# Optimization experiments

Measured on AMD Instinct MI355X. Metric: run time of the kernel, lower is better.

## Reference

```python
import jax, jax.numpy as jnp
import numpy as np

LN_EPS = 1e-5

def layer_norm(x, g, b):
    mu = jnp.mean(x, axis=-1, keepdims=True)
    var = jnp.mean(jnp.square(x - mu), axis=-1, keepdims=True)
    return (x - mu) * jax.lax.rsqrt(var + LN_EPS) * g + b

def ternary_quant(w):
    # BitNet b1.58-style ternary quantization with straight-through estimator
    scale = 1.0 / jnp.clip(jnp.mean(jnp.abs(w)), 1e-5)
    wq = jnp.clip(jnp.round(w * scale), -1.0, 1.0) / scale
    return w + jax.lax.stop_gradient(wq - w)

def setup_inputs() -> dict:
    key = jax.random.key(0)
    ks = jax.random.split(key, 3)
    dim, hidden = 1024, 4096
    B, S = 8, 1024
    x = jax.random.normal(ks[0], (B, S, dim), dtype=jnp.float32)
    w1 = jax.random.normal(ks[1], (hidden, dim), dtype=jnp.float32) * 0.02
    w2 = jax.random.normal(ks[2], (dim, hidden), dtype=jnp.float32) * 0.02
    return {
        "x": x,
        "ln1_g": jnp.ones((dim,), jnp.float32), "ln1_b": jnp.zeros((dim,), jnp.float32),
        "w1": w1, "b1": jnp.zeros((hidden,), jnp.float32),
        "ln2_g": jnp.ones((hidden,), jnp.float32), "ln2_b": jnp.zeros((hidden,), jnp.float32),
        "w2": w2, "b2": jnp.zeros((dim,), jnp.float32),
    }

def reference(x, ln1_g, ln1_b, w1, b1, ln2_g, ln2_b, w2, b2):
    h = layer_norm(x, ln1_g, ln1_b)
    h = jnp.einsum('bsd,hd->bsh', h, ternary_quant(w1)) + b1  # [B,S,hidden]
    h = jax.nn.gelu(h, approximate=False)  # nn.GELU default is exact erf
    h = layer_norm(h, ln2_g, ln2_b)
    out = jnp.einsum('bsh,dh->bsd', h, ternary_quant(w2)) + b2  # [B,S,dim]
    return out
```

## Files before the change

kernel.cpp:

```cpp
#include <hip/hip_runtime.h>
#include <cstdint>
#include <cstddef>

#define DIM   1024
#define HID   4096
#define MROWS 8192

typedef __attribute__((ext_vector_type(8))) __bf16 bf16x8;
typedef __attribute__((ext_vector_type(4))) float  f32x4;
typedef __attribute__((ext_vector_type(4))) int    i32x4;

__device__ __forceinline__ unsigned short f2bf(float f) {
  unsigned int u = __float_as_uint(f);
  u += 0x7fffu + ((u >> 16) & 1u);
  return (unsigned short)(u >> 16);
}
__device__ __forceinline__ float bf2f(unsigned int lo16) {
  return __uint_as_float(lo16 << 16);
}

__device__ __forceinline__ float fast_gelu(float v) {
  float u = v * (0.79788456080286536f + 0.035677408136300125f * v * v);
  float e = __builtin_amdgcn_exp2f(u * 2.8853900817779268f);
  float r = __builtin_amdgcn_rcpf(e + 1.0f);
  return v - v * r;
}

__device__ __forceinline__ void gld16(const void* g, void* l) {
  auto* gp = reinterpret_cast<__attribute__((address_space(1))) unsigned int*>(
      reinterpret_cast<uintptr_t>(g));
  auto* lp = reinterpret_cast<__attribute__((address_space(3))) unsigned int*>(
      reinterpret_cast<uintptr_t>(l));
  __builtin_amdgcn_global_load_lds(gp, lp, 16, 0, 0);
}

__device__ __forceinline__ void wave_reduce2(float& a, float& b) {
#pragma unroll
  for (int off = 32; off > 0; off >>= 1) {
    a += __shfl_xor(a, off, 64);
    b += __shfl_xor(b, off, 64);
  }
}
__device__ __forceinline__ float wave_reduce_max(float m) {
#pragma unroll
  for (int off = 32; off > 0; off >>= 1) m = fmaxf(m, __shfl_xor(m, off, 64));
  return m;
}

__device__ __forceinline__ void block_reduce2(float& a, float& b, int tid) {
  __shared__ float red[8];
  __syncthreads();
  wave_reduce2(a, b);
  if ((tid & 63) == 0) { red[tid >> 6] = a; red[4 + (tid >> 6)] = b; }
  __syncthreads();
  a = red[0] + red[1] + red[2] + red[3];
  b = red[4] + red[5] + red[6] + red[7];
}

__global__ __launch_bounds__(256)
void prep_kernel(const float* __restrict__ w1, const float* __restrict__ w2,
                 float* __restrict__ part,
                 const float* __restrict__ x, const float* __restrict__ g,
                 const float* __restrict__ b, unsigned int* __restrict__ xn8,
                 float* __restrict__ invs) {
  int tid = threadIdx.x;
  int bid = blockIdx.x;
  if (bid < 2048) {
    const float* w = (bid < 1024) ? w1 : w2;
    int blk = bid & 1023;
    const float4* base = (const float4*)w + (size_t)blk * 1024;
    float s = 0.f;
#pragma unroll
    for (int i = 0; i < 4; ++i) {
      float4 v = base[tid + i * 256];
      s += fabsf(v.x) + fabsf(v.y) + fabsf(v.z) + fabsf(v.w);
    }
#pragma unroll
    for (int off = 32; off > 0; off >>= 1) s += __shfl_xor(s, off, 64);
    __shared__ float red[4];
    if ((tid & 63) == 0) red[tid >> 6] = s;
    __syncthreads();
    if (tid == 0) part[bid] = red[0] + red[1] + red[2] + red[3];
  } else {
    const int row  = (bid - 2048) * 4 + (tid >> 6);
    const int lane = tid & 63;
    const float4* xr = (const float4*)(x + (size_t)row * DIM);
    const float4* g4 = (const float4*)g;
    const float4* b4 = (const float4*)b;
    float4 v[4];
    float s = 0.f, ss = 0.f;
#pragma unroll
    for (int p = 0; p < 4; ++p) {
      v[p] = xr[lane + 64 * p];
      s  += v[p].x + v[p].y + v[p].z + v[p].w;
      ss += v[p].x * v[p].x + v[p].y * v[p].y + v[p].z * v[p].z + v[p].w * v[p].w;
    }
    wave_reduce2(s, ss);
    float mu  = s * (1.0f / DIM);
    float var = ss * (1.0f / DIM) - mu * mu;
    float rs  = rsqrtf(var + 1e-5f);
    float n[4][4];
    float amax = 0.f;
#pragma unroll
    for (int p = 0; p < 4; ++p) {
      float4 gg = g4[lane + 64 * p];
      float4 bb = b4[lane + 64 * p];
      n[p][0] = (v[p].x - mu) * rs * gg.x + bb.x;
      n[p][1] = (v[p].y - mu) * rs * gg.y + bb.y;
      n[p][2] = (v[p].z - mu) * rs * gg.z + bb.z;
      n[p][3] = (v[p].w - mu) * rs * gg.w + bb.w;
#pragma unroll
      for (int c = 0; c < 4; ++c) amax = fmaxf(amax, fabsf(n[p][c]));
    }
    amax = wave_reduce_max(amax);
    float sc, iv;
    if (amax < 1e-20f) { sc = 0.f; iv = 0.f; }
    else               { sc = 127.0f / amax; iv = amax * (1.0f / 127.0f); }
    if (lane == 0) invs[row] = iv;
    unsigned int* dst = xn8 + (size_t)row * 256;
#pragma unroll
    for (int p = 0; p < 4; ++p) {
      unsigned r = 0;
#pragma unroll
      for (int c = 0; c < 4; ++c) {
        int q = (int)rintf(n[p][c] * sc);
        r |= ((unsigned)q & 0xffu) << (8 * c);
      }
      dst[lane + 64 * p] = r;
    }
  }
}

__global__ __launch_bounds__(256)
void quant_kernel(const float* __restrict__ part,
                  const float* __restrict__ w1, unsigned int* __restrict__ q1,
                  const float* __restrict__ w2, unsigned short* __restrict__ q2,
                  const float* __restrict__ g2, const float* __restrict__ b2,
                  const float* __restrict__ bias2,
                  float* __restrict__ Sg, float* __restrict__ Cb,
                  float* __restrict__ scal) {
  int bid = blockIdx.x, tid = threadIdx.x;
  const int lane = tid & 63;
  const float4* psrc = (const float4*)(part + ((bid < 512) ? 0 : 1024));
  float a = 0.f, dummy = 0.f;
#pragma unroll
  for (int p = 0; p < 4; ++p) {
    float4 pv = psrc[lane + 64 * p];
    a += pv.x + pv.y + pv.z + pv.w;
  }
  wave_reduce2(a, dummy);
  float mean = fmaxf(a * (1.0f / 4194304.0f), 1e-5f);
  float sc = 1.0f / mean;

  if (bid < 512) {
    if (bid == 0 && tid == 0) scal[0] = mean;
    const int n4 = 1048576;
    int i = bid * 256 + tid;
    for (; i < n4; i += 512 * 256) {
      float4 v = ((const float4*)w1)[i];
      int t0 = (int)fminf(fmaxf(rintf(v.x * sc), -1.f), 1.f);
      int t1 = (int)fminf(fmaxf(rintf(v.y * sc), -1.f), 1.f);
      int t2 = (int)fminf(fmaxf(rintf(v.z * sc), -1.f), 1.f);
      int t3 = (int)fminf(fmaxf(rintf(v.w * sc), -1.f), 1.f);
      unsigned r = ((unsigned)t0 & 0xffu) | (((unsigned)t1 & 0xffu) << 8) |
                   (((unsigned)t2 & 0xffu) << 16) | (((unsigned)t3 & 0xffu) << 24);
      q1[i] = r;
    }
  } else {
    const int d = bid - 512;
    if (d == 0 && tid == 0) scal[1] = mean;
    const float4* wr = (const float4*)(w2 + (size_t)d * HID);
    const float4* g4 = (const float4*)g2;
    const float4* b4 = (const float4*)b2;
    uint2* qr = (uint2*)(q2 + (size_t)d * HID);
    float s1 = 0.f, s2 = 0.f;
#pragma unroll
    for (int i = 0; i < 4; ++i) {
      int idx = tid + 256 * i;
      float4 wv = wr[idx], gv = g4[idx], bv = b4[idx];
      float t0 = fminf(fmaxf(rintf(wv.x * sc), -1.f), 1.f);
      float t1 = fminf(fmaxf(rintf(wv.y * sc), -1.f), 1.f);
      float t2 = fminf(fmaxf(rintf(wv.z * sc), -1.f), 1.f);
      float t3 = fminf(fmaxf(rintf(wv.w * sc), -1.f), 1.f);
      s1 += gv.x * t0 + gv.y * t1 + gv.z * t2 + gv.w * t3;
      s2 += bv.x * t0 + bv.y * t1 + bv.z * t2 + bv.w * t3;
      uint2 r;
      r.x = (unsigned)f2bf(t0 * gv.x) | ((unsigned)f2bf(t1 * gv.y) << 16);
      r.y = (unsigned)f2bf(t2 * gv.z) | ((unsigned)f2bf(t3 * gv.w) << 16);
      qr[idx] = r;
    }
    block_reduce2(s1, s2, tid);
    if (tid == 0) {
      Sg[d] = mean * s1;
      Cb[d] = mean * s2 + bias2[d];
    }
  }
}

__global__ __launch_bounds__(256)
void rowstats_kernel(const unsigned short* __restrict__ h,
                     const float* __restrict__ meanp,
                     float2* __restrict__ murs) {
  const int row  = blockIdx.x * 4 + (threadIdx.x >> 6);
  const int lane = threadIdx.x & 63;
  const uint4* hr = (const uint4*)(h + (size_t)row * HID);
  float s = 0.f, ss = 0.f;
#pragma unroll
  for (int p = 0; p < 8; ++p) {
    uint4 pk = hr[lane + 64 * p];
    const unsigned int* pu = (const unsigned int*)&pk;
#pragma unroll
    for (int j = 0; j < 4; ++j) {
      float lo = bf2f(pu[j] & 0xffffu);
      float hi = __uint_as_float(pu[j] & 0xffff0000u);
      s += lo + hi; ss += lo * lo + hi * hi;
    }
  }
  wave_reduce2(s, ss);
  if (lane == 0) {
    float mu  = s * (1.0f / HID);
    float var = ss * (1.0f / HID) - mu * mu;
    float rs  = rsqrtf(var + 1e-5f);
    murs[row] = make_float2(rs * meanp[1], -rs * mu);
  }
}

__global__ __launch_bounds__(256)
void gemm1_i8(const unsigned char* __restrict__ A,
              const unsigned char* __restrict__ B,
              unsigned short* __restrict__ H,
              const float* __restrict__ wscale_ptr,
              const float* __restrict__ invs,
              const float* __restrict__ bias) {
  __shared__ unsigned char sA[128 * 64];
  __shared__ unsigned char sB[128 * 64];

  const int tid  = threadIdx.x;
  const int lane = tid & 63;
  const int wave = tid >> 6;
  const int wm   = wave & 1;
  const int wn   = wave >> 1;

  const int nbx  = gridDim.x;
  const int id   = blockIdx.y * nbx + blockIdx.x;
  const int xcd  = id & 7;
  const int slot = id >> 3;
  const int bandsPerXcd = gridDim.y >> 3;
  const int band = xcd * bandsPerXcd + slot / nbx;
  const int col  = slot - (slot / nbx) * nbx;
  const int bm   = band * 128;
  const int bn   = col * 128;

  const int csw = ((tid & 3) ^ ((tid >> 3) & 3)) * 16;
  const unsigned char* Ab = A + (size_t)(bm + (tid >> 2)) * 1024 + csw;
  const unsigned char* Bb = B + (size_t)(bn + (tid >> 2)) * 1024 + csw;

  i32x4 acc[4][4] = {};

  const int rowA = (wm * 64 + (lane & 15)) * 64;
  const int rowB = (wn * 64 + (lane & 15)) * 64;
  const int kc = (((lane >> 4) ^ ((lane >> 1) & 3))) * 16;

  for (int k0 = 0; k0 < 1024; k0 += 64) {
    gld16(Ab + k0,              sA + tid * 16);
    gld16(Ab + 64 * 1024 + k0,  sA + 4096 + tid * 16);
    gld16(Bb + k0,              sB + tid * 16);
    gld16(Bb + 64 * 1024 + k0,  sB + 4096 + tid * 16);
    __syncthreads();

    i32x4 af[4], bfr[4];
#pragma unroll
    for (int i = 0; i < 4; ++i) af[i]  = *(const i32x4*)(sA + rowA + i * 1024 + kc);
#pragma unroll
    for (int j = 0; j < 4; ++j) bfr[j] = *(const i32x4*)(sB + rowB + j * 1024 + kc);
#pragma unroll
    for (int i = 0; i < 4; ++i)
#pragma unroll
      for (int j = 0; j < 4; ++j)
        acc[i][j] = __builtin_amdgcn_mfma_i32_16x16x64_i8(af[i], bfr[j], acc[i][j], 0, 0, 0);
    __syncthreads();
  }

  const float wscale = *wscale_ptr;
  float bv[4];
#pragma unroll
  for (int j = 0; j < 4; ++j) bv[j] = bias[bn + wn * 64 + j * 16 + (lane & 15)];
#pragma unroll
  for (int i = 0; i < 4; ++i) {
    const int m0 = bm + wm * 64 + i * 16 + ((lane >> 4) << 2);
    float asc[4];
#pragma unroll
    for (int r = 0; r < 4; ++r) asc[r] = wscale * invs[m0 + r];
#pragma unroll
    for (int j = 0; j < 4; ++j) {
      const int n = bn + wn * 64 + j * 16 + (lane & 15);
#pragma unroll
      for (int r = 0; r < 4; ++r) {
        float v = fast_gelu((float)acc[i][j][r] * asc[r] + bv[j]);
        H[(size_t)(m0 + r) * HID + n] = f2bf(v);
      }
    }
  }
}

template <int MODE, int MT, int KK>
__global__ __launch_bounds__(256)
void gemm_bt(const unsigned short* __restrict__ A,
             const unsigned short* __restrict__ B,
             void* __restrict__ Cv,
             const float* __restrict__ wscale_ptr,
             const float* __restrict__ bias,
             const float2* __restrict__ murs,
             const float* __restrict__ Sg,
             const float* __restrict__ Cb,
             int N) {
  constexpr int IT = MT / 32;
  __shared__ unsigned short sA[MT * 64];
  __shared__ unsigned short sB[128 * 64];

  const int tid  = threadIdx.x;
  const int lane = tid & 63;
  const int wave = tid >> 6;
  const int wm   = wave & 1;
  const int wn   = wave >> 1;

  const int nbx  = gridDim.x;
  const int id   = blockIdx.y * nbx + blockIdx.x;
  const int xcd  = id & 7;
  const int slot = id >> 3;
  const int bandsPerXcd = gridDim.y >> 3;
  const int band = xcd * bandsPerXcd + slot / nbx;
  const int col  = slot - (slot / nbx) * nbx;
  const int bm   = band * MT;
  const int bn   = col * 128;

  const int csw = (((tid & 7) ^ ((tid >> 3) & 7))) * 8;
  const unsigned short* Ab = A + (size_t)(bm + (tid >> 3)) * KK + csw;
  const unsigned short* Bb = B + (size_t)(bn + (tid >> 3)) * KK + csw;

  f32x4 acc[IT][4] = {};

  const int rowA = (wm * (MT / 2) + (lane & 15)) * 64;
  const int rowB = (wn * 64 + (lane & 15)) * 64;
  const int p0 = ((0 + (lane >> 4)) ^ (lane & 7)) * 8;
  const int p1 = ((4 + (lane >> 4)) ^ (lane & 7)) * 8;

  for (int k0 = 0; k0 < KK; k0 += 64) {
#pragma unroll
    for (int i = 0; i < IT; ++i)
      gld16(Ab + (size_t)(32 * i) * KK + k0, sA + i * 2048 + tid * 8);
#pragma unroll
    for (int i = 0; i < 4; ++i)
      gld16(Bb + (size_t)(32 * i) * KK + k0, sB + i * 2048 + tid * 8);
    __syncthreads();

#pragma unroll
    for (int h = 0; h < 2; ++h) {
      const int ph = h ? p1 : p0;
      bf16x8 af[IT], bfr[4];
#pragma unroll
      for (int i = 0; i < IT; ++i) af[i] = *(const bf16x8*)(sA + rowA + i * 1024 + ph);
#pragma unroll
      for (int j = 0; j < 4; ++j) bfr[j] = *(const bf16x8*)(sB + rowB + j * 1024 + ph);
#pragma unroll
      for (int i = 0; i < IT; ++i)
#pragma unroll
        for (int j = 0; j < 4; ++j)
          acc[i][j] = __builtin_amdgcn_mfma_f32_16x16x32_bf16(af[i], bfr[j], acc[i][j], 0, 0, 0);
    }
    __syncthreads();
  }

  if (MODE == 1) {
    const float wscale = *wscale_ptr;
    float bv[4];
#pragma unroll
    for (int j = 0; j < 4; ++j) bv[j] = bias[bn + wn * 64 + j * 16 + (lane & 15)];
#pragma unroll
    for (int i = 0; i < IT; ++i) {
      const int m0 = bm + wm * (MT / 2) + i * 16 + ((lane >> 4) << 2);
#pragma unroll
      for (int j = 0; j < 4; ++j) {
        const int n = bn + wn * 64 + j * 16 + (lane & 15);
#pragma unroll
        for (int r = 0; r < 4; ++r) {
          float v = fast_gelu(acc[i][j][r] * wscale + bv[j]);
          ((unsigned short*)Cv)[(size_t)(m0 + r) * N + n] = f2bf(v);
        }
      }
    }
  } else {
    float sg[4], cb[4];
#pragma unroll
    for (int j = 0; j < 4; ++j) {
      const int n = bn + wn * 64 + j * 16 + (lane & 15);
      sg[j] = Sg[n];
      cb[j] = Cb[n];
    }
#pragma unroll
    for (int i = 0; i < IT; ++i) {
      const int m0 = bm + wm * (MT / 2) + i * 16 + ((lane >> 4) << 2);
#pragma unroll
      for (int r = 0; r < 4; ++r) {
        float2 ab = murs[m0 + r];
#pragma unroll
        for (int j = 0; j < 4; ++j) {
          const int n = bn + wn * 64 + j * 16 + (lane & 15);
          ((float*)Cv)[(size_t)(m0 + r) * N + n] = ab.x * acc[i][j][r] + ab.y * sg[j] + cb[j];
        }
      }
    }
  }
}

extern "C" void kernel_launch(void* const* d_in, const int* in_sizes, int n_in,
                              void* d_out, int out_size, void* d_ws, size_t ws_size,
                              hipStream_t stream) {
  const float* x     = (const float*)d_in[0];
  const float* g1    = (const float*)d_in[1];
  const float* b1v   = (const float*)d_in[2];
  const float* w1    = (const float*)d_in[3];
  const float* bias1 = (const float*)d_in[4];
  const float* g2    = (const float*)d_in[5];
  const float* b2v   = (const float*)d_in[6];
  const float* w2    = (const float*)d_in[7];
  const float* bias2 = (const float*)d_in[8];
  float* out = (float*)d_out;

  char* ws = (char*)d_ws;
  float* scal          = (float*)ws;
  float* part          = (float*)(ws + 64);
  float* invs          = (float*)(ws + 16384);
  unsigned int* q1     = (unsigned int*)(ws + 65536);
  unsigned short* q2   = (unsigned short*)(ws + 65536 + 4194304);
  unsigned int* xn8    = (unsigned int*)((char*)q2 + 8388608);
  unsigned short* h    = (unsigned short*)((char*)xn8 + 8388608);
  float2* murs         = (float2*)((char*)h + 67108864);
  float* Sg            = (float*)(murs + 8192);
  float* Cb            = Sg + 1024;

  prep_kernel<<<4096, 256, 0, stream>>>(w1, w2, part, x, g1, b1v, xn8, invs);
  quant_kernel<<<1536, 256, 0, stream>>>(part, w1, q1, w2, q2, g2, b2v, bias2, Sg, Cb, scal);
  gemm1_i8<<<dim3(HID / 128, MROWS / 128), 256, 0, stream>>>(
      (const unsigned char*)xn8, (const unsigned char*)q1, h, scal + 0, invs, bias1);
  rowstats_kernel<<<2048, 256, 0, stream>>>(h, scal, murs);
  gemm_bt<0, 64, HID><<<dim3(DIM / 128, MROWS / 64), 256, 0, stream>>>(
      h, q2, out, scal + 1, nullptr, murs, Sg, Cb, DIM);
}
```

Baseline: 258.2 us.

## Replace second GEMM with double-buffered 256x128 tile, 8-wave phased pipeline

```diff
diff --git a/kernel.cpp b/kernel.cpp
--- a/kernel.cpp
+++ b/kernel.cpp
@@ -303,111 +303,137 @@
   }
 }
 
-template <int MODE, int MT, int KK>
-__global__ __launch_bounds__(256)
-void gemm_bt(const unsigned short* __restrict__ A,
-             const unsigned short* __restrict__ B,
-             void* __restrict__ Cv,
-             const float* __restrict__ wscale_ptr,
-             const float* __restrict__ bias,
-             const float2* __restrict__ murs,
-             const float* __restrict__ Sg,
-             const float* __restrict__ Cb,
-             int N) {
-  constexpr int IT = MT / 32;
-  __shared__ unsigned short sA[MT * 64];
-  __shared__ unsigned short sB[128 * 64];
+__global__ __launch_bounds__(512, 2)
+void gemm2_8ph(const unsigned short* __restrict__ A,
+               const unsigned short* __restrict__ B,
+               float* __restrict__ C,
+               const float2* __restrict__ murs,
+               const float* __restrict__ Sg,
+               const float* __restrict__ Cb) {
+  __shared__ unsigned short sA[2][256 * 64];
+  __shared__ unsigned short sB[2][128 * 64];
 
   const int tid  = threadIdx.x;
   const int lane = tid & 63;
   const int wave = tid >> 6;
-  const int wm   = wave & 1;
-  const int wn   = wave >> 1;
-
-  const int nbx  = gridDim.x;
-  const int id   = blockIdx.y * nbx + blockIdx.x;
+  const int wm   = wave >> 1;
+  const int wn   = wave & 1;
+
+  const int id   = blockIdx.y * 8 + blockIdx.x;
   const int xcd  = id & 7;
   const int slot = id >> 3;
-  const int bandsPerXcd = gridDim.y >> 3;
-  const int band = xcd * bandsPerXcd + slot / nbx;
-  const int col  = slot - (slot / nbx) * nbx;
-  const int bm   = band * MT;
+  const int band = xcd * 4 + (slot >> 3);
+  const int col  = slot & 7;
+  const int bm   = band * 256;
   const int bn   = col * 128;
 
-  const int csw = (((tid & 7) ^ ((tid >> 3) & 7))) * 8;
-  const unsigned short* Ab = A + (size_t)(bm + (tid >> 3)) * KK + csw;
-  const unsigned short* Bb = B + (size_t)(bn + (tid >> 3)) * KK + csw;
-
-  f32x4 acc[IT][4] = {};
-
-  const int rowA = (wm * (MT / 2) + (lane & 15)) * 64;
-  const int rowB = (wn * 64 + (lane & 15)) * 64;
-  const int p0 = ((0 + (lane >> 4)) ^ (lane & 7)) * 8;
-  const int p1 = ((4 + (lane >> 4)) ^ (lane & 7)) * 8;
-
-  for (int k0 = 0; k0 < KK; k0 += 64) {
-#pragma unroll
-    for (int i = 0; i < IT; ++i)
-      gld16(Ab + (size_t)(32 * i) * KK + k0, sA + i * 2048 + tid * 8);
-#pragma unroll
-    for (int i = 0; i < 4; ++i)
-      gld16(Bb + (size_t)(32 * i) * KK + k0, sB + i * 2048 + tid * 8);
-    __syncthreads();
-
-#pragma unroll
-    for (int h = 0; h < 2; ++h) {
-      const int ph = h ? p1 : p0;
-      bf16x8 af[IT], bfr[4];
-#pragma unroll
-      for (int i = 0; i < IT; ++i) af[i] = *(const bf16x8*)(sA + rowA + i * 1024 + ph);
-#pragma unroll
-      for (int j = 0; j < 4; ++j) bfr[j] = *(const bf16x8*)(sB + rowB + j * 1024 + ph);
-#pragma unroll
-      for (int i = 0; i < IT; ++i)
-#pragma unroll
-        for (int j = 0; j < 4; ++j)
-          acc[i][j] = __builtin_amdgcn_mfma_f32_16x16x32_bf16(af[i], bfr[j], acc[i][j], 0, 0, 0);
-    }
-    __syncthreads();
-  }
-
-  if (MODE == 1) {
-    const float wscale = *wscale_ptr;
-    float bv[4];
-#pragma unroll
-    for (int j = 0; j < 4; ++j) bv[j] = bias[bn + wn * 64 + j * 16 + (lane & 15)];
-#pragma unroll
-    for (int i = 0; i < IT; ++i) {
-      const int m0 = bm + wm * (MT / 2) + i * 16 + ((lane >> 4) << 2);
+  const int csw = ((tid & 7) ^ ((tid >> 3) & 7)) << 3;
+  const unsigned short* Ab = A + (size_t)(bm + (tid >> 3)) * 4096 + csw;
+  const unsigned short* Bb = B + (size_t)(bn + (tid >> 3)) * 4096 + csw;
+  char* la0 = (char*)&sA[0][0] + tid * 16;
+  char* la1 = (char*)&sA[1][0] + tid * 16;
+  char* lb0 = (char*)&sB[0][0] + tid * 16;
+  char* lb1 = (char*)&sB[1][0] + tid * 16;
+
+  const int rowAb = (wm * 64 + (lane & 15)) * 128;
+  const int rowBb = (wn * 64 + (lane & 15)) * 128;
+  const int hi    = lane >> 4;
+  const int ck0   = ((hi)     ^ (lane & 7)) << 4;
+  const int ck1   = ((hi + 4) ^ (lane & 7)) << 4;
+
+  f32x4 acc[4][4] = {};
+
+#pragma unroll
+  for (int i = 0; i < 4; ++i) gld16(Ab + (size_t)i * 262144, la0 + i * 8192);
+#pragma unroll
+  for (int i = 0; i < 2; ++i) gld16(Bb + (size_t)i * 262144, lb0 + i * 8192);
+#pragma unroll
+  for (int i = 0; i < 4; ++i) gld16(Ab + (size_t)i * 262144 + 64, la1 + i * 8192);
+  asm volatile("s_waitcnt vmcnt(4)" ::: "memory");
+  __builtin_amdgcn_s_barrier();
+
+#define Q8(IA, JB)                                                                 \
+  do {                                                                             \
+    __builtin_amdgcn_s_setprio(1);                                                 \
+    _Pragma("unroll") for (int ii = 0; ii < 2; ++ii)                               \
+    _Pragma("unroll") for (int jj = 0; jj < 2; ++jj)                               \
+    _Pragma("unroll") for (int kk = 0; kk < 2; ++kk)                               \
+      acc[IA + ii][JB + jj] = __builtin_amdgcn_mfma_f32_16x16x32_bf16(             \
+          af[IA + ii][kk], bfr[JB + jj][kk], acc[IA + ii][JB + jj], 0, 0, 0);      \
+    __builtin_amdgcn_s_setprio(0);                                                 \
+  } while (0)
+
+  for (int t = 0; t < 64; ++t) {
+    const int cur = t & 1;
+    const char* a = (const char*)&sA[0][0] + cur * 32768;
+    const char* b = (const char*)&sB[0][0] + cur * 16384;
+    char* lbP = cur ? lb0 : lb1;
+    char* laC = cur ? la1 : la0;
+    const size_t kB1 = (t + 1 < 64) ? (size_t)(t + 1) * 64 : 0;
+    const size_t kA2 = (t + 2 < 64) ? (size_t)(t + 2) * 64 : 0;
+
+    bf16x8 af[4][2], bfr[4][2];
+
+    af[0][0]  = *(const bf16x8*)(a + rowAb + 0 * 2048 + ck0);
+    af[0][1]  = *(const bf16x8*)(a + rowAb + 0 * 2048 + ck1);
+    af[1][0]  = *(const bf16x8*)(a + rowAb + 1 * 2048 + ck0);
+    af[1][1]  = *(const bf16x8*)(a + rowAb + 1 * 2048 + ck1);
+    bfr[0][0] = *(const bf16x8*)(b + rowBb + 0 * 2048 + ck0);
+    bfr[0][1] = *(const bf16x8*)(b + rowBb + 0 * 2048 + ck1);
+    bfr[1][0] = *(const bf16x8*)(b + rowBb + 1 * 2048 + ck0);
+    bfr[1][1] = *(const bf16x8*)(b + rowBb + 1 * 2048 + ck1);
+#pragma unroll
+    for (int i = 0; i < 2; ++i) gld16(Bb + (size_t)i * 262144 + kB1, lbP + i * 8192);
+    __builtin_amdgcn_s_barrier();
+    asm volatile("s_waitcnt lgkmcnt(0)" ::: "memory");
+    Q8(0, 0);
+    __builtin_amdgcn_s_barrier();
+
+    bfr[2][0] = *(const bf16x8*)(b + rowBb + 2 * 2048 + ck0);
+    bfr[2][1] = *(const bf16x8*)(b + rowBb + 2 * 2048 + ck1);
+    bfr[3][0] = *(const bf16x8*)(b + rowBb + 3 * 2048 + ck0);
+    bfr[3][1] = *(const bf16x8*)(b + rowBb + 3 * 2048 + ck1);
+    __builtin_amdgcn_s_barrier();
+    asm volatile("s_waitcnt lgkmcnt(0)" ::: "memory");
+    Q8(0, 2);
+    __builtin_amdgcn_s_barrier();
+
+    af[2][0] = *(const bf16x8*)(a + rowAb + 2 * 2048 + ck0);
+    af[2][1] = *(const bf16x8*)(a + rowAb + 2 * 2048 + ck1);
+    af[3][0] = *(const bf16x8*)(a + rowAb + 3 * 2048 + ck0);
+    af[3][1] = *(const bf16x8*)(a + rowAb + 3 * 2048 + ck1);
+    __builtin_amdgcn_s_barrier();
+    asm volatile("s_waitcnt lgkmcnt(0)" ::: "memory");
+    Q8(2, 0);
+    __builtin_amdgcn_s_barrier();
+
+#pragma unroll
+    for (int i = 0; i < 4; ++i) gld16(Ab + (size_t)i * 262144 + kA2, laC + i * 8192);
+    Q8(2, 2);
+    asm volatile("s_waitcnt vmcnt(4)" ::: "memory");
+    __builtin_amdgcn_s_barrier();
+  }
+#undef Q8
+
+  asm volatile("s_waitcnt vmcnt(0)" ::: "memory");
+
+  float sg[4], cb[4];
+#pragma unroll
+  for (int j = 0; j < 4; ++j) {
+    const int n = bn + wn * 64 + j * 16 + (lane & 15);
+    sg[j] = Sg[n];
+    cb[j] = Cb[n];
+  }
+#pragma unroll
+  for (int i = 0; i < 4; ++i) {
+    const int m0 = bm + wm * 64 + i * 16 + (hi << 2);
+#pragma unroll
+    for (int r = 0; r < 4; ++r) {
+      float2 ab = murs[m0 + r];
 #pragma unroll
       for (int j = 0; j < 4; ++j) {
         const int n = bn + wn * 64 + j * 16 + (lane & 15);
-#pragma unroll
-        for (int r = 0; r < 4; ++r) {
-          float v = fast_gelu(acc[i][j][r] * wscale + bv[j]);
-          ((unsigned short*)Cv)[(size_t)(m0 + r) * N + n] = f2bf(v);
-        }
-      }
-    }
-  } else {
-    float sg[4], cb[4];
-#pragma unroll
-    for (int j = 0; j < 4; ++j) {
-      const int n = bn + wn * 64 + j * 16 + (lane & 15);
-      sg[j] = Sg[n];
-      cb[j] = Cb[n];
-    }
-#pragma unroll
-    for (int i = 0; i < IT; ++i) {
-      const int m0 = bm + wm * (MT / 2) + i * 16 + ((lane >> 4) << 2);
-#pragma unroll
-      for (int r = 0; r < 4; ++r) {
-        float2 ab = murs[m0 + r];
-#pragma unroll
-        for (int j = 0; j < 4; ++j) {
-          const int n = bn + wn * 64 + j * 16 + (lane & 15);
-          ((float*)Cv)[(size_t)(m0 + r) * N + n] = ab.x * acc[i][j][r] + ab.y * sg[j] + cb[j];
-        }
+        C[(size_t)(m0 + r) * 1024 + n] = ab.x * acc[i][j][r] + ab.y * sg[j] + cb[j];
       }
     }
   }
@@ -444,6 +470,5 @@
   gemm1_i8<<<dim3(HID / 128, MROWS / 128), 256, 0, stream>>>(
       (const unsigned char*)xn8, (const unsigned char*)q1, h, scal + 0, invs, bias1);
   rowstats_kernel<<<2048, 256, 0, stream>>>(h, scal, murs);
-  gemm_bt<0, 64, HID><<<dim3(DIM / 128, MROWS / 64), 256, 0, stream>>>(
-      h, q2, out, scal + 1, nullptr, murs, Sg, Cb, DIM);
-}
+  gemm2_8ph<<<dim3(8, 32), 512, 0, stream>>>(h, q2, out, murs, Sg, Cb);
+}
```

Result: faster. 248.6 us (-3.7%).
